# Kernel tuning notes

Hardware: AMD Instinct MI355X
Metric: run time of the kernel (lower is better)

## Reference

```python
import jax, jax.numpy as jnp
import numpy as np

B, T, V, D, C = 64, 512, 100000, 256, 20
LN_EPS = 1e-5


def setup_inputs() -> dict:
    key = jax.random.key(0)
    ks = jax.random.split(key, 8)
    words = jax.random.randint(ks[0], (B, T), 0, V)
    seq_len = jax.random.randint(ks[1], (B,), 1, T + 1)  # at least 1 valid token
    target = jax.random.randint(ks[2], (B, T), 0, C)
    emb = jax.random.normal(ks[3], (V, D), jnp.float32) * 0.02
    ln_g = jnp.ones((D,), jnp.float32)
    ln_b = jnp.zeros((D,), jnp.float32)
    W = jax.random.normal(ks[4], (D, C), jnp.float32) * 0.05
    b = jnp.zeros((C,), jnp.float32)
    trans = jax.random.normal(ks[5], (C, C), jnp.float32) * 0.1
    start = jax.random.normal(ks[6], (C,), jnp.float32) * 0.1
    end = jax.random.normal(ks[7], (C,), jnp.float32) * 0.1
    return dict(words=words, seq_len=seq_len, target=target, emb=emb,
                ln_g=ln_g, ln_b=ln_b, W=W, b=b, trans=trans, start=start, end=end)


def _crf_nll(logits, tags, mask, trans, start, end):
    # logits: [B,T,C] log-softmax emissions; tags: [B,T] int; mask: [B,T] bool
    lt = jnp.transpose(logits, (1, 0, 2))  # [T,B,C]
    tt = jnp.transpose(tags)               # [T,B]
    mt = jnp.transpose(mask)               # [T,B]

    # ---- normalizer: forward algorithm (logsumexp recurrence) ----
    alpha0 = lt[0] + start[None, :]        # [B,C], include_start_end_trans

    def step(alpha, x):
        emit, m = x                        # emit: [B,C], m: [B]
        # [B, C_prev, C_next]
        scores = alpha[:, :, None] + trans[None, :, :] + emit[:, None, :]
        new = jax.scipy.special.logsumexp(scores, axis=1)
        return jnp.where(m[:, None], new, alpha), None

    alpha, _ = jax.lax.scan(step, alpha0, (lt[1:], mt[1:]))
    normalizer = jax.scipy.special.logsumexp(alpha + end[None, :], axis=-1)  # [B]

    # ---- gold score ----
    mf = mt.astype(logits.dtype)
    emit_sc = jnp.take_along_axis(lt, tt[:, :, None], axis=2)[:, :, 0]  # [T,B]
    emit_sum = jnp.sum(emit_sc * mf, axis=0)                            # [B]
    tr_sc = trans[tt[:-1], tt[1:]]                                      # [T-1,B]
    tr_sum = jnp.sum(tr_sc * mf[1:], axis=0)                            # [B]
    last = jnp.sum(mt.astype(jnp.int32), axis=0) - 1                    # [B]
    gold = emit_sum + tr_sum + start[tt[0]] + end[tt[last, jnp.arange(tt.shape[1])]]
    return normalizer - gold  # per-sequence NLL, [B]


def reference(words, seq_len, target, emb, ln_g, ln_b, W, b, trans, start, end):
    x = emb[words]                                      # [B,T,D] embedding gather
    mu = jnp.mean(x, axis=-1, keepdims=True)
    var = jnp.mean((x - mu) ** 2, axis=-1, keepdims=True)
    x = (x - mu) * jax.lax.rsqrt(var + LN_EPS) * ln_g + ln_b  # LayerNorm
    feats = x @ W + b                                   # [B,T,C]
    # dropout p=0.0 -> identity
    logits = jax.nn.log_softmax(feats, axis=-1)
    mask = jnp.arange(T)[None, :] < seq_len[:, None]    # seq_len_to_mask
    nll = _crf_nll(logits, target, mask, trans, start, end)
    return jnp.mean(nll)
```

## Files before the change

### kernel.cpp

```cpp
#include <hip/hip_runtime.h>
#include <math.h>

#define BB 64
#define TT 512
#define DD 256
#define CC 20
#define SS 32
#define LL 16
#define WW 16
#define PR 20
#define NSEG (BB * SS)
#define LN_EPS 1e-5f

__device__ __forceinline__ float dpp_sum16(float v) {
  v += __int_as_float(__builtin_amdgcn_update_dpp(0, __float_as_int(v), 0xB1, 0xF, 0xF, true));
  v += __int_as_float(__builtin_amdgcn_update_dpp(0, __float_as_int(v), 0x4E, 0xF, 0xF, true));
  v += __int_as_float(__builtin_amdgcn_update_dpp(0, __float_as_int(v), 0x141, 0xF, 0xF, true));
  v += __int_as_float(__builtin_amdgcn_update_dpp(0, __float_as_int(v), 0x140, 0xF, 0xF, true));
  return v;
}
__device__ __forceinline__ float dpp_max16(float v) {
  v = fmaxf(v, __int_as_float(__builtin_amdgcn_update_dpp(0, __float_as_int(v), 0xB1, 0xF, 0xF, true)));
  v = fmaxf(v, __int_as_float(__builtin_amdgcn_update_dpp(0, __float_as_int(v), 0x4E, 0xF, 0xF, true)));
  v = fmaxf(v, __int_as_float(__builtin_amdgcn_update_dpp(0, __float_as_int(v), 0x141, 0xF, 0xF, true)));
  v = fmaxf(v, __int_as_float(__builtin_amdgcn_update_dpp(0, __float_as_int(v), 0x140, 0xF, 0xF, true)));
  return v;
}
__device__ __forceinline__ float wave_reduce_sum64(float v) {
  #pragma unroll
  for (int off = 32; off > 0; off >>= 1) v += __shfl_xor(v, off, 64);
  return v;
}
__device__ __forceinline__ float wave_reduce_max64(float v) {
  #pragma unroll
  for (int off = 32; off > 0; off >>= 1) v = fmaxf(v, __shfl_xor(v, off, 64));
  return v;
}

__global__ __launch_bounds__(256, 1) void token_probs_kernel(
    const int* __restrict__ words, const float* __restrict__ emb,
    const float* __restrict__ ln_g, const float* __restrict__ ln_b,
    const float* __restrict__ W, const float* __restrict__ bias,
    const int* __restrict__ seq_len, const int* __restrict__ target,
    const float* __restrict__ trans, const float* __restrict__ startv,
    const float* __restrict__ endv,
    float* __restrict__ probs, float* __restrict__ goldEmit)
{
  int b = blockIdx.x >> 5;
  int t0 = (blockIdx.x & 31) << 4;
  int len = seq_len[b];
  if (t0 >= len) return;

  __shared__ __align__(16) float4 sW4[64 * 21];
  __shared__ float sb[CC];
  int tid = threadIdx.x;
  for (int ei = tid; ei < 64 * CC; ei += 256) {
    int d4 = ei / CC, c = ei - d4 * CC;
    int base = 4 * d4 * CC + c;
    sW4[d4 * 21 + c] = make_float4(W[base], W[base + CC], W[base + 2 * CC], W[base + 3 * CC]);
  }
  if (tid < CC) sb[tid] = bias[tid];
  __syncthreads();

  int l = tid & 15;
  int t = t0 + (tid >> 4);
  if (t >= len) return;
  int token = (b << 9) + t;

  int word = words[token];
  const float4* row = (const float4*)(emb + (size_t)word * DD);
  float4 x0 = row[l], x1 = row[l + 16], x2 = row[l + 32], x3 = row[l + 48];

  float4 g0 = ((const float4*)ln_g)[l];
  float4 g1 = ((const float4*)ln_g)[l + 16];
  float4 g2 = ((const float4*)ln_g)[l + 32];
  float4 g3 = ((const float4*)ln_g)[l + 48];
  float4 e0v = ((const float4*)ln_b)[l];
  float4 e1v = ((const float4*)ln_b)[l + 16];
  float4 e2v = ((const float4*)ln_b)[l + 32];
  float4 e3v = ((const float4*)ln_b)[l + 48];

  float s1 = (x0.x + x0.y) + (x0.z + x0.w) + (x1.x + x1.y) + (x1.z + x1.w)
           + (x2.x + x2.y) + (x2.z + x2.w) + (x3.x + x3.y) + (x3.z + x3.w);
  float s2 = x0.x*x0.x + x0.y*x0.y + x0.z*x0.z + x0.w*x0.w
           + x1.x*x1.x + x1.y*x1.y + x1.z*x1.z + x1.w*x1.w
           + x2.x*x2.x + x2.y*x2.y + x2.z*x2.z + x2.w*x2.w
           + x3.x*x3.x + x3.y*x3.y + x3.z*x3.z + x3.w*x3.w;
  s1 = dpp_sum16(s1);
  s2 = dpp_sum16(s2);
  float mu = s1 * (1.f / DD);
  float var = s2 * (1.f / DD) - mu * mu;
  float rr = rsqrtf(var + LN_EPS);

  x0.x = (x0.x - mu) * rr * g0.x + e0v.x;  x0.y = (x0.y - mu) * rr * g0.y + e0v.y;
  x0.z = (x0.z - mu) * rr * g0.z + e0v.z;  x0.w = (x0.w - mu) * rr * g0.w + e0v.w;
  x1.x = (x1.x - mu) * rr * g1.x + e1v.x;  x1.y = (x1.y - mu) * rr * g1.y + e1v.y;
  x1.z = (x1.z - mu) * rr * g1.z + e1v.z;  x1.w = (x1.w - mu) * rr * g1.w + e1v.w;
  x2.x = (x2.x - mu) * rr * g2.x + e2v.x;  x2.y = (x2.y - mu) * rr * g2.y + e2v.y;
  x2.z = (x2.z - mu) * rr * g2.z + e2v.z;  x2.w = (x2.w - mu) * rr * g2.w + e2v.w;
  x3.x = (x3.x - mu) * rr * g3.x + e3v.x;  x3.y = (x3.y - mu) * rr * g3.y + e3v.y;
  x3.z = (x3.z - mu) * rr * g3.z + e3v.z;  x3.w = (x3.w - mu) * rr * g3.w + e3v.w;

  int tgt = target[token];
  float f0 = 0.f, f1 = 0.f;
  float ftgt = 0.f;
  #pragma unroll
  for (int c = 0; c < CC; ++c) {
    float4 w0 = sW4[l * 21 + c];
    float4 w1 = sW4[(l + 16) * 21 + c];
    float4 w2 = sW4[(l + 32) * 21 + c];
    float4 w3 = sW4[(l + 48) * 21 + c];
    float pp = (x0.x*w0.x + x0.y*w0.y) + (x0.z*w0.z + x0.w*w0.w)
             + (x1.x*w1.x + x1.y*w1.y) + (x1.z*w1.z + x1.w*w1.w)
             + (x2.x*w2.x + x2.y*w2.y) + (x2.z*w2.z + x2.w*w2.w)
             + (x3.x*w3.x + x3.y*w3.y) + (x3.z*w3.z + x3.w*w3.w);
    pp = dpp_sum16(pp) + sb[c];
    if (c < 16) { if (l == c) f0 = pp; }
    else        { if (l == c - 16) f1 = pp; }
    if (c < 16) { if (l == c && tgt == c) ftgt = pp; }
    else        { if (l == c - 16 && tgt == c) ftgt = pp; }
  }

  float m = f0;
  if (l < 4) m = fmaxf(m, f1);
  m = dpp_max16(m);
  float q0 = __expf(f0 - m);
  float q1 = (l < 4) ? __expf(f1 - m) : 0.f;
  float ssum = dpp_sum16(q0 + q1);
  float inv = 1.0f / ssum;
  float lsm = m + __logf(ssum);
  ftgt = dpp_sum16(ftgt);

  float* pt = probs + (size_t)token * PR;
  pt[l] = q0 * inv;
  if (l < 4) pt[16 + l] = q1 * inv;

  if (l == 0) {
    float g = ftgt - lsm;
    if (t > 0) g += trans[target[token - 1] * CC + tgt];
    else       g += startv[tgt];
    if (t == len - 1) g += endv[tgt];
    goldEmit[token] = g;
  }
}

__global__ __launch_bounds__(64, 1) void segment_kernel(
    const float* __restrict__ probs, const int* __restrict__ seq_len,
    const float* __restrict__ trans, const float* __restrict__ startv,
    float* __restrict__ partialZ, float* __restrict__ finalA)
{
  int tid = threadIdx.x;
  int grp = tid / 20;
  int l = tid - grp * 20;
  int chain = blockIdx.x * 3 + grp;
  bool act = (grp < 3) && (chain < NSEG);
  int ch = act ? chain : 0;
  int b = ch >> 5;
  int s = ch & (SS - 1);
  int len = seq_len[b];
  int base = act ? grp * 20 : 0;

  int prod_start = s * LL + 1;
  int prod_end   = min(s * LL + LL, len - 1);
  bool empty = prod_start > prod_end;

  if (__ballot(act && !empty) == 0ull) {
    if (act && l == 0) partialZ[ch] = 0.f;
    return;
  }

  float E0  = __expf(trans[0*CC + l]),  E1  = __expf(trans[1*CC + l]);
  float E2  = __expf(trans[2*CC + l]),  E3  = __expf(trans[3*CC + l]);
  float E4  = __expf(trans[4*CC + l]),  E5  = __expf(trans[5*CC + l]);
  float E6  = __expf(trans[6*CC + l]),  E7  = __expf(trans[7*CC + l]);
  float E8  = __expf(trans[8*CC + l]),  E9  = __expf(trans[9*CC + l]);
  float E10 = __expf(trans[10*CC + l]), E11 = __expf(trans[11*CC + l]);
  float E12 = __expf(trans[12*CC + l]), E13 = __expf(trans[13*CC + l]);
  float E14 = __expf(trans[14*CC + l]), E15 = __expf(trans[15*CC + l]);
  float E16 = __expf(trans[16*CC + l]), E17 = __expf(trans[17*CC + l]);
  float E18 = __expf(trans[18*CC + l]), E19 = __expf(trans[19*CC + l]);

  const float* pb = probs + (size_t)b * TT * PR + l;

  float v = (s == 0) ? pb[0] * __expf(startv[l]) : 1.0f;

#define STEP(t) do {                                            \
    float pr = pb[(t) * PR];                                    \
    float a0, a1, a2, a3;                                       \
    a0  = __shfl(v, base + 0, 64) * E0;                         \
    a1  = __shfl(v, base + 1, 64) * E1;                         \
    a2  = __shfl(v, base + 2, 64) * E2;                         \
    a3  = __shfl(v, base + 3, 64) * E3;                         \
    a0 += __shfl(v, base + 4, 64) * E4;                         \
    a1 += __shfl(v, base + 5, 64) * E5;                         \
    a2 += __shfl(v, base + 6, 64) * E6;                         \
    a3 += __shfl(v, base + 7, 64) * E7;                         \
    a0 += __shfl(v, base + 8, 64) * E8;                         \
    a1 += __shfl(v, base + 9, 64) * E9;                         \
    a2 += __shfl(v, base + 10, 64) * E10;                       \
    a3 += __shfl(v, base + 11, 64) * E11;                       \
    a0 += __shfl(v, base + 12, 64) * E12;                       \
    a1 += __shfl(v, base + 13, 64) * E13;                       \
    a2 += __shfl(v, base + 14, 64) * E14;                       \
    a3 += __shfl(v, base + 15, 64) * E15;                       \
    a0 += __shfl(v, base + 16, 64) * E16;                       \
    a1 += __shfl(v, base + 17, 64) * E17;                       \
    a2 += __shfl(v, base + 18, 64) * E18;                       \
    a3 += __shfl(v, base + 19, 64) * E19;                       \
    v = ((a0 + a1) + (a2 + a3)) * pr;                           \
  } while (0)

  int nwarm = (s == 0 || empty) ? 0 : WW;
  for (int t = prod_start - nwarm; t < prod_start; ++t) STEP(t);

  __shared__ float sv[64];
  sv[tid] = v;
  __syncthreads();
  float Smid = 0.f;
  #pragma unroll
  for (int i = 0; i < CC; ++i) Smid += sv[base + i];
  __syncthreads();

  if (!empty) {
    for (int t = prod_start; t <= prod_end; ++t) STEP(t);
  }
#undef STEP

  sv[tid] = v;
  __syncthreads();
  float Send = 0.f;
  #pragma unroll
  for (int i = 0; i < CC; ++i) Send += sv[base + i];

  if (act) {
    float pz;
    if (empty)       pz = 0.f;
    else if (s == 0) pz = __logf(Send);
    else             pz = __logf(Send) - __logf(Smid);
    if (l == 0) partialZ[ch] = pz;
    if (!empty && s == (len - 2) / LL)
      finalA[b * CC + l] = v / Send;
  }
}

__global__ __launch_bounds__(64, 1) void combine_kernel(
    const float* __restrict__ probs, const float* __restrict__ partialZ,
    const float* __restrict__ finalA, const float* __restrict__ goldEmit,
    const int* __restrict__ seq_len, const float* __restrict__ startv,
    const float* __restrict__ endv, float* __restrict__ nll)
{
  int b = blockIdx.x;
  int j = threadIdx.x;
  int len = seq_len[b];

  float gsum = 0.f;
  const float* ge = goldEmit + ((size_t)b << 9);
  for (int t = j; t < len; t += 64) gsum += ge[t];
  gsum = wave_reduce_sum64(gsum);

  float Z;
  if (len == 1) {
    const float* pb = probs + (size_t)b * TT * PR;
    float val = (j < CC) ? __logf(pb[j]) + startv[j] + endv[j] : -INFINITY;
    float m = wave_reduce_max64(val);
    float ssum = wave_reduce_sum64((j < CC) ? __expf(val - m) : 0.f);
    Z = m + __logf(ssum);
  } else {
    float pz = (j < SS) ? partialZ[b * SS + j] : 0.f;
    pz = wave_reduce_sum64(pz);
    float ve = (j < CC) ? finalA[b * CC + j] * __expf(endv[j]) : 0.f;
    float ssum = wave_reduce_sum64(ve);
    Z = pz + __logf(ssum);
  }

  if (j == 0) nll[b] = Z - gsum;
}

__global__ __launch_bounds__(64) void mean_kernel(
    const float* __restrict__ nll, float* __restrict__ out)
{
  float v = nll[threadIdx.x];
  v = wave_reduce_sum64(v);
  if (threadIdx.x == 0) out[0] = v * (1.0f / BB);
}

extern "C" void kernel_launch(void* const* d_in, const int* in_sizes, int n_in,
                              void* d_out, int out_size, void* d_ws, size_t ws_size,
                              hipStream_t stream) {
  const int*   words   = (const int*)d_in[0];
  const int*   seq_len = (const int*)d_in[1];
  const int*   target  = (const int*)d_in[2];
  const float* emb     = (const float*)d_in[3];
  const float* ln_g    = (const float*)d_in[4];
  const float* ln_b    = (const float*)d_in[5];
  const float* W       = (const float*)d_in[6];
  const float* bias    = (const float*)d_in[7];
  const float* trans   = (const float*)d_in[8];
  const float* startv  = (const float*)d_in[9];
  const float* endv    = (const float*)d_in[10];

  float* probs    = (float*)d_ws;
  float* goldEmit = probs + (size_t)BB * TT * PR;
  float* partialZ = goldEmit + (size_t)BB * TT;
  float* finalA   = partialZ + NSEG;
  float* nll      = finalA + BB * CC;
  float* out      = (float*)d_out;

  token_probs_kernel<<<2048, 256, 0, stream>>>(words, emb, ln_g, ln_b, W, bias,
                                               seq_len, target, trans, startv,
                                               endv, probs, goldEmit);
  segment_kernel<<<(NSEG + 2) / 3, 64, 0, stream>>>(probs, seq_len, trans,
                                                    startv, partialZ, finalA);
  combine_kernel<<<BB, 64, 0, stream>>>(probs, partialZ, finalA, goldEmit,
                                        seq_len, startv, endv, nll);
  mean_kernel<<<1, 64, 0, stream>>>(nll, out);
}
```

Before: 178.1 us.

## Fuse combine and mean into segment kernel via last-block atomic counter

Per-token gold scores are now accumulated straight into a per-sequence sum with atomicAdd, so the goldEmit buffer is no longer needed. The separate combine and mean kernels are folded into the segment kernel: each chain bumps a global counter, and the wave that finishes last computes every sequence's normalizer and the mean loss. This cuts two kernel launches and their gaps but adds a memset, atomic traffic and a serial per-thread tail in the final wave. Float atomics also make the gold sum order nondeterministic.

```diff
diff --git a/kernel.cpp b/kernel.cpp
--- a/kernel.cpp
+++ b/kernel.cpp
@@ -31,11 +31,6 @@
   for (int off = 32; off > 0; off >>= 1) v += __shfl_xor(v, off, 64);
   return v;
 }
-__device__ __forceinline__ float wave_reduce_max64(float v) {
-  #pragma unroll
-  for (int off = 32; off > 0; off >>= 1) v = fmaxf(v, __shfl_xor(v, off, 64));
-  return v;
-}
 
 __global__ __launch_bounds__(256, 1) void token_probs_kernel(
     const int* __restrict__ words, const float* __restrict__ emb,
@@ -44,7 +39,7 @@
     const int* __restrict__ seq_len, const int* __restrict__ target,
     const float* __restrict__ trans, const float* __restrict__ startv,
     const float* __restrict__ endv,
-    float* __restrict__ probs, float* __restrict__ goldEmit)
+    float* __restrict__ probs, float* __restrict__ gsum)
 {
   int b = blockIdx.x >> 5;
   int t0 = (blockIdx.x & 31) << 4;
@@ -140,14 +135,17 @@
     if (t > 0) g += trans[target[token - 1] * CC + tgt];
     else       g += startv[tgt];
     if (t == len - 1) g += endv[tgt];
-    goldEmit[token] = g;
-  }
-}
-
-__global__ __launch_bounds__(64, 1) void segment_kernel(
+    atomicAdd(&gsum[b], g);
+  }
+}
+
+__global__ __launch_bounds__(64, 1) void segment_finalize_kernel(
     const float* __restrict__ probs, const int* __restrict__ seq_len,
     const float* __restrict__ trans, const float* __restrict__ startv,
-    float* __restrict__ partialZ, float* __restrict__ finalA)
+    const float* __restrict__ endv,
+    float* __restrict__ partialZ, float* __restrict__ finalA,
+    const float* __restrict__ gsum, int* __restrict__ cntAll,
+    float* __restrict__ out)
 {
   int tid = threadIdx.x;
   int grp = tid / 20;
@@ -164,25 +162,21 @@
   int prod_end   = min(s * LL + LL, len - 1);
   bool empty = prod_start > prod_end;
 
-  if (__ballot(act && !empty) == 0ull) {
-    if (act && l == 0) partialZ[ch] = 0.f;
-    return;
-  }
-
-  float E0  = __expf(trans[0*CC + l]),  E1  = __expf(trans[1*CC + l]);
-  float E2  = __expf(trans[2*CC + l]),  E3  = __expf(trans[3*CC + l]);
-  float E4  = __expf(trans[4*CC + l]),  E5  = __expf(trans[5*CC + l]);
-  float E6  = __expf(trans[6*CC + l]),  E7  = __expf(trans[7*CC + l]);
-  float E8  = __expf(trans[8*CC + l]),  E9  = __expf(trans[9*CC + l]);
-  float E10 = __expf(trans[10*CC + l]), E11 = __expf(trans[11*CC + l]);
-  float E12 = __expf(trans[12*CC + l]), E13 = __expf(trans[13*CC + l]);
-  float E14 = __expf(trans[14*CC + l]), E15 = __expf(trans[15*CC + l]);
-  float E16 = __expf(trans[16*CC + l]), E17 = __expf(trans[17*CC + l]);
-  float E18 = __expf(trans[18*CC + l]), E19 = __expf(trans[19*CC + l]);
-
-  const float* pb = probs + (size_t)b * TT * PR + l;
-
-  float v = (s == 0) ? pb[0] * __expf(startv[l]) : 1.0f;
+  float pz = 0.f;
+  if (__ballot(act && !empty) != 0ull) {
+    float E0  = __expf(trans[0*CC + l]),  E1  = __expf(trans[1*CC + l]);
+    float E2  = __expf(trans[2*CC + l]),  E3  = __expf(trans[3*CC + l]);
+    float E4  = __expf(trans[4*CC + l]),  E5  = __expf(trans[5*CC + l]);
+    float E6  = __expf(trans[6*CC + l]),  E7  = __expf(trans[7*CC + l]);
+    float E8  = __expf(trans[8*CC + l]),  E9  = __expf(trans[9*CC + l]);
+    float E10 = __expf(trans[10*CC + l]), E11 = __expf(trans[11*CC + l]);
+    float E12 = __expf(trans[12*CC + l]), E13 = __expf(trans[13*CC + l]);
+    float E14 = __expf(trans[14*CC + l]), E15 = __expf(trans[15*CC + l]);
+    float E16 = __expf(trans[16*CC + l]), E17 = __expf(trans[17*CC + l]);
+    float E18 = __expf(trans[18*CC + l]), E19 = __expf(trans[19*CC + l]);
+
+    const float* pb = probs + (size_t)b * TT * PR + l;
+    float v = (s == 0) ? pb[0] * __expf(startv[l]) : 1.0f;
 
 #define STEP(t) do {                                            \
     float pr = pb[(t) * PR];                                    \
@@ -210,78 +204,66 @@
     v = ((a0 + a1) + (a2 + a3)) * pr;                           \
   } while (0)
 
-  int nwarm = (s == 0 || empty) ? 0 : WW;
-  for (int t = prod_start - nwarm; t < prod_start; ++t) STEP(t);
-
-  __shared__ float sv[64];
-  sv[tid] = v;
-  __syncthreads();
-  float Smid = 0.f;
-  #pragma unroll
-  for (int i = 0; i < CC; ++i) Smid += sv[base + i];
-  __syncthreads();
-
-  if (!empty) {
-    for (int t = prod_start; t <= prod_end; ++t) STEP(t);
-  }
+    int nwarm = (s == 0 || empty) ? 0 : WW;
+    for (int t = prod_start - nwarm; t < prod_start; ++t) STEP(t);
+
+    __shared__ float sv[64];
+    sv[tid] = v;
+    __syncthreads();
+    float Smid = 0.f;
+    #pragma unroll
+    for (int i = 0; i < CC; ++i) Smid += sv[base + i];
+    __syncthreads();
+
+    if (!empty) {
+      for (int t = prod_start; t <= prod_end; ++t) STEP(t);
+    }
 #undef STEP
 
-  sv[tid] = v;
-  __syncthreads();
-  float Send = 0.f;
-  #pragma unroll
-  for (int i = 0; i < CC; ++i) Send += sv[base + i];
-
-  if (act) {
-    float pz;
-    if (empty)       pz = 0.f;
-    else if (s == 0) pz = __logf(Send);
-    else             pz = __logf(Send) - __logf(Smid);
-    if (l == 0) partialZ[ch] = pz;
-    if (!empty && s == (len - 2) / LL)
-      finalA[b * CC + l] = v / Send;
-  }
-}
-
-__global__ __launch_bounds__(64, 1) void combine_kernel(
-    const float* __restrict__ probs, const float* __restrict__ partialZ,
-    const float* __restrict__ finalA, const float* __restrict__ goldEmit,
-    const int* __restrict__ seq_len, const float* __restrict__ startv,
-    const float* __restrict__ endv, float* __restrict__ nll)
-{
-  int b = blockIdx.x;
-  int j = threadIdx.x;
-  int len = seq_len[b];
-
-  float gsum = 0.f;
-  const float* ge = goldEmit + ((size_t)b << 9);
-  for (int t = j; t < len; t += 64) gsum += ge[t];
-  gsum = wave_reduce_sum64(gsum);
-
-  float Z;
-  if (len == 1) {
-    const float* pb = probs + (size_t)b * TT * PR;
-    float val = (j < CC) ? __logf(pb[j]) + startv[j] + endv[j] : -INFINITY;
-    float m = wave_reduce_max64(val);
-    float ssum = wave_reduce_sum64((j < CC) ? __expf(val - m) : 0.f);
-    Z = m + __logf(ssum);
-  } else {
-    float pz = (j < SS) ? partialZ[b * SS + j] : 0.f;
-    pz = wave_reduce_sum64(pz);
-    float ve = (j < CC) ? finalA[b * CC + j] * __expf(endv[j]) : 0.f;
-    float ssum = wave_reduce_sum64(ve);
-    Z = pz + __logf(ssum);
-  }
-
-  if (j == 0) nll[b] = Z - gsum;
-}
-
-__global__ __launch_bounds__(64) void mean_kernel(
-    const float* __restrict__ nll, float* __restrict__ out)
-{
-  float v = nll[threadIdx.x];
-  v = wave_reduce_sum64(v);
-  if (threadIdx.x == 0) out[0] = v * (1.0f / BB);
+    sv[tid] = v;
+    __syncthreads();
+    float Send = 0.f;
+    #pragma unroll
+    for (int i = 0; i < CC; ++i) Send += sv[base + i];
+
+    if (act && !empty) {
+      pz = (s == 0) ? __logf(Send) : __logf(Send) - __logf(Smid);
+      if (s == (len - 2) / LL)
+        finalA[b * CC + l] = v / Send;
+    }
+  }
+
+  if (act && l == 0) partialZ[ch] = pz;
+
+  __threadfence();
+  int oldc = -1;
+  if (act && l == 0) oldc = atomicAdd(cntAll, 1);
+
+  if (__ballot(oldc == NSEG - 1) != 0ull) {
+    __threadfence();
+    int j = tid;
+    int lj = seq_len[j];
+    float Z;
+    if (lj == 1) {
+      const float* pbj = probs + (size_t)j * TT * PR;
+      float mm = -INFINITY, sum = 0.f;
+      for (int c = 0; c < CC; ++c) {
+        float vv = __logf(pbj[c]) + startv[c] + endv[c];
+        if (vv > mm) { sum = sum * __expf(mm - vv) + 1.f; mm = vv; }
+        else sum += __expf(vv - mm);
+      }
+      Z = mm + __logf(sum);
+    } else {
+      float ps = 0.f;
+      for (int s2 = 0; s2 < SS; ++s2) ps += partialZ[j * SS + s2];
+      float se = 0.f;
+      for (int c = 0; c < CC; ++c) se += finalA[j * CC + c] * __expf(endv[c]);
+      Z = ps + __logf(se);
+    }
+    float nl = Z - gsum[j];
+    nl = wave_reduce_sum64(nl);
+    if (tid == 0) out[0] = nl * (1.0f / BB);
+  }
 }
 
 extern "C" void kernel_launch(void* const* d_in, const int* in_sizes, int n_in,
@@ -300,18 +282,17 @@
   const float* endv    = (const float*)d_in[10];
 
   float* probs    = (float*)d_ws;
-  float* goldEmit = probs + (size_t)BB * TT * PR;
-  float* partialZ = goldEmit + (size_t)BB * TT;
+  float* partialZ = probs + (size_t)BB * TT * PR;
   float* finalA   = partialZ + NSEG;
-  float* nll      = finalA + BB * CC;
+  float* gsum     = finalA + BB * CC;
+  int*   cntAll   = (int*)(gsum + BB);
   float* out      = (float*)d_out;
+
+  hipMemsetAsync(gsum, 0, (BB + 1) * sizeof(float), stream);
 
   token_probs_kernel<<<2048, 256, 0, stream>>>(words, emb, ln_g, ln_b, W, bias,
                                                seq_len, target, trans, startv,
-                                               endv, probs, goldEmit);
-  segment_kernel<<<(NSEG + 2) / 3, 64, 0, stream>>>(probs, seq_len, trans,
-                                                    startv, partialZ, finalA);
-  combine_kernel<<<BB, 64, 0, stream>>>(probs, partialZ, finalA, goldEmit,
-                                        seq_len, startv, endv, nll);
-  mean_kernel<<<1, 64, 0, stream>>>(nll, out);
-}
+                                               endv, probs, gsum);
+  segment_finalize_kernel<<<(NSEG + 2) / 3, 64, 0, stream>>>(
+      probs, seq_len, trans, startv, endv, partialZ, finalA, gsum, cntAll, out);
+}
```

New measurement: 212.3 us. +19.2%, slower.
